# Kernel tuning notes

Measured on AMD Instinct MI355X. Metric: run time of the kernel, lower is better.

## Reference

```python
import jax, jax.numpy as jnp
import numpy as np

N = 50000
E = 800000
IN = 3
H = 64
OUT = 128
L = 4


def _layernorm(x, w, b, eps=1e-5):
    mu = jnp.mean(x, axis=-1, keepdims=True)
    var = jnp.mean(jnp.square(x - mu), axis=-1, keepdims=True)
    return (x - mu) * jax.lax.rsqrt(var + eps) * w + b


def setup_inputs() -> dict:
    key = jax.random.key(0)
    ks = jax.random.split(key, 12)

    def lin(k, fan_in, shape):
        return jax.random.normal(k, shape, dtype=jnp.float32) / np.sqrt(fan_in)

    x = jax.random.normal(ks[0], (N, IN), dtype=jnp.float32)
    edge_index = jax.random.randint(ks[1], (2, E), 0, N, dtype=jnp.int32)
    return {
        "x": x,
        "edge_index": edge_index,
        "in_w": lin(ks[2], IN, (IN, H)), "in_b": jnp.zeros((H,), jnp.float32),
        "ew1": lin(ks[3], 2, (2, H)), "eb1": jnp.zeros((H,), jnp.float32),
        "ew2": lin(ks[4], H, (H, H)), "eb2": jnp.zeros((H,), jnp.float32),
        "cw1": lin(ks[5], H, (L, H, H)), "cb1": jnp.zeros((L, H), jnp.float32),
        "cw2": lin(ks[6], H, (L, H, H)), "cb2": jnp.zeros((L, H), jnp.float32),
        "lnw": jnp.ones((L, H), jnp.float32), "lnb": jnp.zeros((L, H), jnp.float32),
        "fw": lin(ks[7], H, (H, OUT)), "fb": jnp.zeros((OUT,), jnp.float32),
        "rw": lin(ks[8], H, (H, OUT)), "rb": jnp.zeros((OUT,), jnp.float32),
        "ow": jnp.ones((OUT,), jnp.float32), "ob": jnp.zeros((OUT,), jnp.float32),
    }


def reference(x, edge_index, in_w, in_b, ew1, eb1, ew2, eb2,
              cw1, cb1, cw2, cb2, lnw, lnb, fw, fb, rw, rb, ow, ob):
    pos = x[:, :2]
    row, col = edge_index[0], edge_index[1]  # source, target (PyG convention)
    rel_pos = pos[col] - pos[row]                              # [E, 2]
    edge_attr = jnp.maximum(rel_pos @ ew1 + eb1, 0.0) @ ew2 + eb2  # [E, H]

    h = x @ in_w + in_b  # [N, H]
    for i in range(L):
        identity = h
        # GINEConv (eps=0): mlp(x_i + sum_j relu(x_j + e_ij))
        msg = jax.nn.relu(h[row] + edge_attr)                  # [E, H]
        agg = jax.ops.segment_sum(msg, col, num_segments=N)    # [N, H]
        m = h + agg
        m = jnp.maximum(m @ cw1[i] + cb1[i], 0.0) @ cw2[i] + cb2[i]
        m = _layernorm(m, lnw[i], lnb[i])
        h = jax.nn.gelu(m, approximate=False) + identity

    out = (h @ fw + fb) + (h @ rw + rb)
    return _layernorm(out, ow, ob)
```

## Files before the change

kernel.cpp:

```cpp
#include <hip/hip_runtime.h>
#include <hip/hip_fp16.h>
#include <stdint.h>

#define NN 50000
#define NE 800000
#define SCAN_BLOCKS 196

typedef _Float16 half8v __attribute__((ext_vector_type(8)));
typedef float f32x4 __attribute__((ext_vector_type(4)));

static __device__ __forceinline__ __half2 u2h2(unsigned int u) {
    union { unsigned int u; __half2 h; } c; c.u = u; return c.h;
}
static __device__ __forceinline__ unsigned int h22u(__half2 h) {
    union { __half2 h; unsigned int u; } c; c.h = h; return c.u;
}

static __device__ __forceinline__ float4 fma4(float4 a, float s, float4 w) {
    a.x = fmaf(s, w.x, a.x); a.y = fmaf(s, w.y, a.y);
    a.z = fmaf(s, w.z, a.z); a.w = fmaf(s, w.w, a.w);
    return a;
}
static __device__ __forceinline__ void acc8(float* acc, float4 hv, float4 ev) {
    const unsigned int* hu = (const unsigned int*)&hv;
    const unsigned int* eu = (const unsigned int*)&ev;
    #pragma unroll
    for (int q = 0; q < 4; ++q) {
        float2 hf = __half22float2(u2h2(hu[q]));
        float2 ef = __half22float2(u2h2(eu[q]));
        acc[q * 2]     += fmaxf(hf.x + ef.x, 0.f);
        acc[q * 2 + 1] += fmaxf(hf.y + ef.y, 0.f);
    }
}

__global__ __launch_bounds__(256) void k_deg(const int* __restrict__ ei, int* __restrict__ offcur) {
    int e = blockIdx.x * 256 + threadIdx.x;
    atomicAdd(&offcur[ei[NE + e]], 1);
}

__global__ __launch_bounds__(256) void k_scanA(const int* __restrict__ off, int* __restrict__ part) {
    __shared__ int s[256];
    int t = threadIdx.x;
    int idx = blockIdx.x * 256 + t;
    int d = (idx < NN) ? off[idx] : 0;
    s[t] = d; __syncthreads();
    for (int o = 128; o > 0; o >>= 1) {
        if (t < o) s[t] += s[t + o];
        __syncthreads();
    }
    if (t == 0) part[blockIdx.x] = s[0];
}

__global__ __launch_bounds__(256) void k_scanB(int* __restrict__ part) {
    __shared__ int s[256];
    int t = threadIdx.x;
    int d = (t < SCAN_BLOCKS) ? part[t] : 0;
    s[t] = d; __syncthreads();
    #pragma unroll
    for (int o = 1; o < 256; o <<= 1) {
        int v = (t >= o) ? s[t - o] : 0;
        __syncthreads();
        s[t] += v;
        __syncthreads();
    }
    if (t < SCAN_BLOCKS) part[t] = s[t] - d;
}

__global__ __launch_bounds__(256) void k_scanC(int* __restrict__ off, const int* __restrict__ part) {
    __shared__ int s[256];
    int t = threadIdx.x;
    int idx = blockIdx.x * 256 + t;
    int d = (idx < NN) ? off[idx] : 0;
    s[t] = d; __syncthreads();
    #pragma unroll
    for (int o = 1; o < 256; o <<= 1) {
        int v = (t >= o) ? s[t - o] : 0;
        __syncthreads();
        s[t] += v;
        __syncthreads();
    }
    if (idx < NN) off[idx] = s[t] - d + part[blockIdx.x];
}

__global__ __launch_bounds__(256) void k_prep(const float* __restrict__ ew2,
        const float* __restrict__ cw1, const float* __restrict__ cw2,
        __half* __restrict__ wf) {
    int b = blockIdx.x;
    const float* src;
    if (b == 0) src = ew2;
    else {
        int l = (b - 1) >> 1;
        src = ((b - 1) & 1) ? (cw2 + (size_t)l * 4096) : (cw1 + (size_t)l * 4096);
    }
    __half* dst = wf + (size_t)b * 4096;
    int tid = threadIdx.x;
    for (int i = tid; i < 4096; i += 256) {
        int k = i >> 6, n = i & 63;
        int kt = k >> 5, kin = k & 31;
        int quad = kin >> 3, j = kin & 7;
        int nt = n >> 4, nin = n & 15;
        dst[(size_t)((kt * 4 + nt) * 64 + quad * 16 + nin) * 8 + j] = __float2half(src[i]);
    }
}

__global__ __launch_bounds__(256) void k_input(const float* __restrict__ x,
        const float* __restrict__ in_w, const float* __restrict__ in_b,
        __half* __restrict__ Ah) {
    int n = blockIdx.x * 4 + (threadIdx.x >> 6);
    int k = threadIdx.x & 63;
    const float* xr = x + (size_t)n * 3;
    float v = in_b[k] + xr[0] * in_w[k] + xr[1] * in_w[64 + k] + xr[2] * in_w[128 + k];
    Ah[(size_t)n * 64 + k] = __float2half(v);
}

__global__ __launch_bounds__(256) void k_edge(const float* __restrict__ x,
        const int* __restrict__ ei,
        const float* __restrict__ ew1, const float* __restrict__ eb1,
        const float* __restrict__ eb2, const __half* __restrict__ w2f,
        int* __restrict__ offcur, unsigned short* __restrict__ rows,
        __half* __restrict__ ea) {
    __shared__ float s_w1[128], s_b1[64], s_b2[64];
    __shared__ float s_rx[256], s_ry[256];
    __shared__ int s_pos[256];
    __shared__ __half s_d[4][16][80];
    int tid = threadIdx.x, lane = tid & 63, w = tid >> 6;

    half8v bf[8];
    {
        const half8v* W2F = (const half8v*)w2f;
        #pragma unroll
        for (int f = 0; f < 8; ++f) bf[f] = W2F[f * 64 + lane];
    }
    if (tid < 128) s_w1[tid] = ew1[tid];
    if (tid < 64) s_b1[tid] = eb1[tid];
    else if (tid < 128) s_b2[tid - 64] = eb2[tid - 64];
    int eb = blockIdx.x * 256;
    int my_r, my_pos;
    {
        int e = eb + tid;
        int r = ei[e], c = ei[NE + e];
        s_rx[tid] = x[(size_t)c * 3]     - x[(size_t)r * 3];
        s_ry[tid] = x[(size_t)c * 3 + 1] - x[(size_t)r * 3 + 1];
        int pos = atomicAdd(&offcur[c], 1);
        my_r = r; my_pos = pos;
        s_pos[tid] = pos;
    }
    __syncthreads();

    int lm = lane & 15, lq = lane >> 4;
    #pragma unroll
    for (int t = 0; t < 4; ++t) {
        int ebase = w * 64 + t * 16;
        float rx = s_rx[ebase + lm], ry = s_ry[ebase + lm];
        half8v a0, a1;
        #pragma unroll
        for (int j = 0; j < 8; ++j) {
            int k0 = lq * 8 + j;
            a0[j] = (_Float16)fmaxf(fmaf(rx, s_w1[k0], fmaf(ry, s_w1[64 + k0], s_b1[k0])), 0.f);
            int k1 = k0 + 32;
            a1[j] = (_Float16)fmaxf(fmaf(rx, s_w1[k1], fmaf(ry, s_w1[64 + k1], s_b1[k1])), 0.f);
        }
        f32x4 acc[4];
        #pragma unroll
        for (int nt = 0; nt < 4; ++nt) {
            float b = s_b2[nt * 16 + lm];
            acc[nt][0] = b; acc[nt][1] = b; acc[nt][2] = b; acc[nt][3] = b;
            acc[nt] = __builtin_amdgcn_mfma_f32_16x16x32_f16(a0, bf[nt],     acc[nt], 0, 0, 0);
            acc[nt] = __builtin_amdgcn_mfma_f32_16x16x32_f16(a1, bf[4 + nt], acc[nt], 0, 0, 0);
        }
        __builtin_amdgcn_wave_barrier();
        #pragma unroll
        for (int nt = 0; nt < 4; ++nt)
            #pragma unroll
            for (int r = 0; r < 4; ++r)
                s_d[w][lq * 4 + r][nt * 16 + lm] = __float2half(acc[nt][r]);
        __builtin_amdgcn_wave_barrier();
        int row = lane >> 2, seg = lane & 3;
        int pos = s_pos[w * 64 + t * 16 + row];
        uint4 v0 = *(const uint4*)&s_d[w][row][seg * 16];
        uint4 v1 = *(const uint4*)&s_d[w][row][seg * 16 + 8];
        uint4* dst = (uint4*)&ea[(size_t)pos * 64 + seg * 16];
        dst[0] = v0;
        dst[1] = v1;
        __builtin_amdgcn_wave_barrier();
    }
    rows[my_pos] = (unsigned short)my_r;
}

__global__ __launch_bounds__(256) void k_agg(const __half* __restrict__ Ah,
        const __half* __restrict__ ea, const unsigned short* __restrict__ rows,
        const int* __restrict__ offcur, __half* __restrict__ M) {
    const float4* A4 = (const float4*)Ah;
    const float4* E4 = (const float4*)ea;
    int w = threadIdx.x >> 6, lane = threadIdx.x & 63;
    int es = lane >> 3, oc = lane & 7;
    int n = blockIdx.x * 4 + w;
    int p0 = (n == 0) ? 0 : offcur[n - 1];
    int p1 = offcur[n];
    float acc[8] = {0,0,0,0,0,0,0,0};
    float accB[8] = {0,0,0,0,0,0,0,0};
    for (int base = p0; base < p1; base += 64) {
        int cnt = min(64, p1 - base);
        int rl = (int)rows[base + min(lane, cnt - 1)];
        int j = 0;
        for (; j + 16 <= cnt; j += 16) {
            int i0 = j + es, i1 = j + 8 + es;
            int r0 = __shfl(rl, i0, 64);
            int r1 = __shfl(rl, i1, 64);
            float4 h0 = A4[(size_t)r0 * 8 + oc];
            float4 h1 = A4[(size_t)r1 * 8 + oc];
            float4 e0 = E4[(size_t)(base + i0) * 8 + oc];
            float4 e1 = E4[(size_t)(base + i1) * 8 + oc];
            acc8(acc, h0, e0);
            acc8(accB, h1, e1);
        }
        for (; j < cnt; j += 8) {
            int i0 = j + es;
            bool valid = i0 < cnt;
            int ic = valid ? i0 : (cnt - 1);
            int r0 = __shfl(rl, ic, 64);
            float4 h0 = A4[(size_t)r0 * 8 + oc];
            float4 e0 = E4[(size_t)(base + ic) * 8 + oc];
            if (valid) acc8(acc, h0, e0);
        }
    }
    #pragma unroll
    for (int q = 0; q < 8; ++q) acc[q] += accB[q];
    #pragma unroll
    for (int m = 8; m < 64; m <<= 1) {
        #pragma unroll
        for (int q = 0; q < 8; ++q) acc[q] += __shfl_xor(acc[q], m, 64);
    }
    if (es == 0) {
        float4 sv = A4[(size_t)n * 8 + oc];
        const unsigned int* su = (const unsigned int*)&sv;
        unsigned int o[4];
        #pragma unroll
        for (int q = 0; q < 4; ++q) {
            float2 sf = __half22float2(u2h2(su[q]));
            o[q] = h22u(__floats2half2_rn(sf.x + acc[q * 2], sf.y + acc[q * 2 + 1]));
        }
        *(uint4*)&M[(size_t)n * 64 + oc * 8] = *(uint4*)&o[0];
    }
}

__global__ __launch_bounds__(256) void k_node(__half* __restrict__ Ah, const __half* __restrict__ M,
        const __half* __restrict__ w1f, const __half* __restrict__ w2f,
        const float* __restrict__ cb1, const float* __restrict__ cb2,
        const float* __restrict__ lnw, const float* __restrict__ lnb) {
    __shared__ __half s_u[4][16][72];
    __shared__ float s_b1[64], s_b2[64], s_g[64], s_bt[64];
    int tid = threadIdx.x, lane = tid & 63, w = tid >> 6;
    int lm = lane & 15, lq = lane >> 4;

    half8v bw1[8], bw2[8];
    {
        const half8v* W1F = (const half8v*)w1f;
        const half8v* W2F = (const half8v*)w2f;
        #pragma unroll
        for (int f = 0; f < 8; ++f) { bw1[f] = W1F[f * 64 + lane]; bw2[f] = W2F[f * 64 + lane]; }
    }
    if (tid < 64) { s_b1[tid] = cb1[tid]; s_g[tid] = lnw[tid]; }
    else if (tid < 128) { s_b2[tid - 64] = cb2[tid - 64]; s_bt[tid - 64] = lnb[tid - 64]; }
    __syncthreads();

    int nb = blockIdx.x * 64;
    int na = nb + w * 16 + lm;
    int nac = min(na, NN - 1);

    const uint4* M4 = (const uint4*)M;
    uint4 a0u = M4[(size_t)nac * 8 + lq];
    uint4 a1u = M4[(size_t)nac * 8 + 4 + lq];
    half8v a0 = *(const half8v*)&a0u;
    half8v a1 = *(const half8v*)&a1u;

    f32x4 acc[4];
    #pragma unroll
    for (int nt = 0; nt < 4; ++nt) {
        float b = s_b1[nt * 16 + lm];
        acc[nt][0] = b; acc[nt][1] = b; acc[nt][2] = b; acc[nt][3] = b;
        acc[nt] = __builtin_amdgcn_mfma_f32_16x16x32_f16(a0, bw1[nt],     acc[nt], 0, 0, 0);
        acc[nt] = __builtin_amdgcn_mfma_f32_16x16x32_f16(a1, bw1[4 + nt], acc[nt], 0, 0, 0);
    }
    __builtin_amdgcn_wave_barrier();
    #pragma unroll
    for (int nt = 0; nt < 4; ++nt)
        #pragma unroll
        for (int r = 0; r < 4; ++r)
            s_u[w][lq * 4 + r][nt * 16 + lm] = __float2half(fmaxf(acc[nt][r], 0.f));
    __builtin_amdgcn_wave_barrier();

    half8v u0 = *(const half8v*)&s_u[w][lm][lq * 8];
    half8v u1 = *(const half8v*)&s_u[w][lm][32 + lq * 8];
    #pragma unroll
    for (int nt = 0; nt < 4; ++nt) {
        float b = s_b2[nt * 16 + lm];
        acc[nt][0] = b; acc[nt][1] = b; acc[nt][2] = b; acc[nt][3] = b;
        acc[nt] = __builtin_amdgcn_mfma_f32_16x16x32_f16(u0, bw2[nt],     acc[nt], 0, 0, 0);
        acc[nt] = __builtin_amdgcn_mfma_f32_16x16x32_f16(u1, bw2[4 + nt], acc[nt], 0, 0, 0);
    }

    float S[4], SQ[4];
    #pragma unroll
    for (int r = 0; r < 4; ++r) {
        S[r]  = acc[0][r] + acc[1][r] + acc[2][r] + acc[3][r];
        SQ[r] = acc[0][r] * acc[0][r] + acc[1][r] * acc[1][r]
              + acc[2][r] * acc[2][r] + acc[3][r] * acc[3][r];
    }
    #pragma unroll
    for (int m = 1; m < 16; m <<= 1) {
        #pragma unroll
        for (int r = 0; r < 4; ++r) {
            S[r]  += __shfl_xor(S[r], m, 64);
            SQ[r] += __shfl_xor(SQ[r], m, 64);
        }
    }
    __builtin_amdgcn_wave_barrier();
    #pragma unroll
    for (int r = 0; r < 4; ++r) {
        float mu  = S[r] * (1.f / 64.f);
        float var = SQ[r] * (1.f / 64.f) - mu * mu;
        float rs  = rsqrtf(var + 1e-5f);
        #pragma unroll
        for (int nt = 0; nt < 4; ++nt) {
            int c = nt * 16 + lm;
            float y = (acc[nt][r] - mu) * rs * s_g[c] + s_bt[c];
            float ge = 0.5f * y * (1.f + erff(y * 0.70710678118654752f));
            s_u[w][lq * 4 + r][c] = __float2half(ge);
        }
    }
    __builtin_amdgcn_wave_barrier();

    #pragma unroll
    for (int it = 0; it < 2; ++it) {
        int ck = lq + 4 * it;
        int n = nb + w * 16 + lm;
        if (n < NN) {
            uint4 ge8 = *(const uint4*)&s_u[w][lm][ck * 8];
            uint4 id8 = *(const uint4*)&Ah[(size_t)n * 64 + ck * 8];
            const unsigned int* gu = (const unsigned int*)&ge8;
            const unsigned int* iu = (const unsigned int*)&id8;
            unsigned int o[4];
            #pragma unroll
            for (int p = 0; p < 4; ++p) {
                float2 gf = __half22float2(u2h2(gu[p]));
                float2 iff = __half22float2(u2h2(iu[p]));
                o[p] = h22u(__floats2half2_rn(gf.x + iff.x, gf.y + iff.y));
            }
            *(uint4*)&Ah[(size_t)n * 64 + ck * 8] = *(uint4*)&o[0];
        }
    }
}

__global__ __launch_bounds__(256) void k_final(const __half* __restrict__ Ah,
        const float* __restrict__ fw, const float* __restrict__ fb,
        const float* __restrict__ rw, const float* __restrict__ rb,
        const float* __restrict__ ow, const float* __restrict__ ob,
        float* __restrict__ out) {
    __shared__ float s_W[64 * 128];
    __shared__ float s_h[32 * 68];
    __shared__ float s_b[128];
    __shared__ float s_red[32][4];
    int tid = threadIdx.x;
    for (int i = tid; i < 8192; i += 256) s_W[i] = fw[i] + rw[i];
    if (tid < 128) s_b[tid] = fb[tid] + rb[tid];
    int nb = blockIdx.x * 32;
    for (int i = tid; i < 2048; i += 256) {
        int nl = i >> 6, k = i & 63;
        int n = nb + nl;
        s_h[nl * 68 + k] = (n < NN) ? __half2float(Ah[(size_t)n * 64 + k]) : 0.f;
    }
    __syncthreads();

    int lane = tid & 63, w = tid >> 6;
    int chh = w & 1, nh = w >> 1;
    int cq = lane & 15, ng = lane >> 4;
    int c0 = chh * 64 + cq * 4;
    int rbase = nh * 16 + ng * 4;

    float4 acc[4];
    {
        float4 bq = *(const float4*)&s_b[c0];
        acc[0] = bq; acc[1] = bq; acc[2] = bq; acc[3] = bq;
    }
    #pragma unroll 4
    for (int k4 = 0; k4 < 16; ++k4) {
        float4 m0 = *(const float4*)&s_h[(rbase + 0) * 68 + k4 * 4];
        float4 m1 = *(const float4*)&s_h[(rbase + 1) * 68 + k4 * 4];
        float4 m2 = *(const float4*)&s_h[(rbase + 2) * 68 + k4 * 4];
        float4 m3 = *(const float4*)&s_h[(rbase + 3) * 68 + k4 * 4];
        #pragma unroll
        for (int kk = 0; kk < 4; ++kk) {
            float4 w4 = *(const float4*)&s_W[(k4 * 4 + kk) * 128 + c0];
            acc[0] = fma4(acc[0], ((const float*)&m0)[kk], w4);
            acc[1] = fma4(acc[1], ((const float*)&m1)[kk], w4);
            acc[2] = fma4(acc[2], ((const float*)&m2)[kk], w4);
            acc[3] = fma4(acc[3], ((const float*)&m3)[kk], w4);
        }
    }
    #pragma unroll
    for (int j = 0; j < 4; ++j) {
        float4 v = acc[j];
        float sum = v.x + v.y + v.z + v.w;
        float sq  = v.x * v.x + v.y * v.y + v.z * v.z + v.w * v.w;
        #pragma unroll
        for (int m = 1; m < 16; m <<= 1) {
            sum += __shfl_xor(sum, m, 64);
            sq  += __shfl_xor(sq, m, 64);
        }
        if (cq == 0) {
            s_red[rbase + j][chh * 2]     = sum;
            s_red[rbase + j][chh * 2 + 1] = sq;
        }
    }
    __syncthreads();
    float4 gq = *(const float4*)&ow[c0];
    float4 bq = *(const float4*)&ob[c0];
    #pragma unroll
    for (int j = 0; j < 4; ++j) {
        int nl = rbase + j;
        int n = nb + nl;
        float tsum = s_red[nl][0] + s_red[nl][2];
        float tsq  = s_red[nl][1] + s_red[nl][3];
        float mu  = tsum * (1.f / 128.f);
        float var = tsq * (1.f / 128.f) - mu * mu;
        float rs  = rsqrtf(var + 1e-5f);
        if (n < NN) {
            float4 v = acc[j];
            float4 o;
            o.x = (v.x - mu) * rs * gq.x + bq.x;
            o.y = (v.y - mu) * rs * gq.y + bq.y;
            o.z = (v.z - mu) * rs * gq.z + bq.z;
            o.w = (v.w - mu) * rs * gq.w + bq.w;
            *(float4*)&out[(size_t)n * 128 + c0] = o;
        }
    }
}

extern "C" void kernel_launch(void* const* d_in, const int* in_sizes, int n_in,
                              void* d_out, int out_size, void* d_ws, size_t ws_size,
                              hipStream_t stream) {
    const float* x    = (const float*)d_in[0];
    const int*   ei   = (const int*)d_in[1];
    const float* in_w = (const float*)d_in[2];
    const float* in_b = (const float*)d_in[3];
    const float* ew1  = (const float*)d_in[4];
    const float* eb1  = (const float*)d_in[5];
    const float* ew2  = (const float*)d_in[6];
    const float* eb2  = (const float*)d_in[7];
    const float* cw1  = (const float*)d_in[8];
    const float* cb1  = (const float*)d_in[9];
    const float* cw2  = (const float*)d_in[10];
    const float* cb2  = (const float*)d_in[11];
    const float* lnw  = (const float*)d_in[12];
    const float* lnb  = (const float*)d_in[13];
    const float* fw   = (const float*)d_in[14];
    const float* fb   = (const float*)d_in[15];
    const float* rw   = (const float*)d_in[16];
    const float* rb   = (const float*)d_in[17];
    const float* ow   = (const float*)d_in[18];
    const float* ob   = (const float*)d_in[19];
    float* out = (float*)d_out;

    char* ws = (char*)d_ws;
    __half*         ea   = (__half*)ws;
    __half*         Ah   = (__half*)(ws + 102400000);
    unsigned short* rows = (unsigned short*)(ws + 108800000);
    int*            off  = (int*)(ws + 110400000);
    __half*         M    = (__half*)(ws + 110600016);
    __half*         wf   = (__half*)(ws + 117000016);
    int*            part = (int*)M;

    (void)hipMemsetAsync(off, 0, (NN + 1) * sizeof(int), stream);
    k_deg<<<NE / 256, 256, 0, stream>>>(ei, off);
    k_scanA<<<SCAN_BLOCKS, 256, 0, stream>>>(off, part);
    k_scanB<<<1, 256, 0, stream>>>(part);
    k_scanC<<<SCAN_BLOCKS, 256, 0, stream>>>(off, part);
    k_prep<<<9, 256, 0, stream>>>(ew2, cw1, cw2, wf);
    k_input<<<NN / 4, 256, 0, stream>>>(x, in_w, in_b, Ah);
    k_edge<<<NE / 256, 256, 0, stream>>>(x, ei, ew1, eb1, eb2, wf, off, rows, ea);

    const int nodeBlocks = (NN + 63) / 64;
    for (int l = 0; l < 4; ++l) {
        k_agg<<<NN / 4, 256, 0, stream>>>(Ah, ea, rows, off, M);
        k_node<<<nodeBlocks, 256, 0, stream>>>(Ah, M,
            wf + (size_t)(1 + 2 * l) * 4096, wf + (size_t)(2 + 2 * l) * 4096,
            cb1 + (size_t)l * 64, cb2 + (size_t)l * 64,
            lnw + (size_t)l * 64, lnb + (size_t)l * 64);
    }
    k_final<<<(NN + 31) / 32, 256, 0, stream>>>(Ah, fw, fb, rw, rb, ow, ob, out);
}
```

Measured before the change: 406.4 us.

## Recompute edge MLP inside aggregation instead of materializing edge features

Replaces the precomputed 800k×64 fp16 edge-attribute buffer with a compact per-edge record (source row plus fp16 relative position) and recomputes the edge MLP with MFMA inside each aggregation pass. This removes the write of roughly 100 MB of edge features and its re-read in each of the four layers, trading memory traffic for repeated MFMA compute. The aggregation now processes edges in chunks of 16 per wave, with fewer edges in flight per iteration. Storing relative positions in fp16 adds a small precision loss.

```diff
diff --git a/kernel.cpp b/kernel.cpp
--- a/kernel.cpp
+++ b/kernel.cpp
@@ -14,6 +14,12 @@
 }
 static __device__ __forceinline__ unsigned int h22u(__half2 h) {
     union { __half2 h; unsigned int u; } c; c.h = h; return c.u;
+}
+static __device__ __forceinline__ float us2f(unsigned short s) {
+    union { unsigned short s; __half h; } c; c.s = s; return __half2float(c.h);
+}
+static __device__ __forceinline__ unsigned short f2us(float f) {
+    union { __half h; unsigned short s; } c; c.h = __float2half(f); return c.s;
 }
 
 static __device__ __forceinline__ float4 fma4(float4 a, float s, float4 w) {
@@ -113,17 +119,34 @@
     Ah[(size_t)n * 64 + k] = __float2half(v);
 }
 
-__global__ __launch_bounds__(256) void k_edge(const float* __restrict__ x,
-        const int* __restrict__ ei,
+__global__ __launch_bounds__(256) void k_rel(const float* __restrict__ x,
+        const int* __restrict__ ei, int* __restrict__ offcur,
+        ushort4* __restrict__ rec) {
+    int e = blockIdx.x * 256 + threadIdx.x;
+    int r = ei[e], c = ei[NE + e];
+    float rx = x[(size_t)c * 3]     - x[(size_t)r * 3];
+    float ry = x[(size_t)c * 3 + 1] - x[(size_t)r * 3 + 1];
+    int pos = atomicAdd(&offcur[c], 1);
+    ushort4 rc;
+    rc.x = (unsigned short)r;
+    rc.y = f2us(rx);
+    rc.z = f2us(ry);
+    rc.w = 0;
+    rec[pos] = rc;
+}
+
+__global__ __launch_bounds__(256) void k_agg(const __half* __restrict__ Ah,
+        const ushort4* __restrict__ rec, const int* __restrict__ offcur,
+        const __half* __restrict__ w2f,
         const float* __restrict__ ew1, const float* __restrict__ eb1,
-        const float* __restrict__ eb2, const __half* __restrict__ w2f,
-        int* __restrict__ offcur, unsigned short* __restrict__ rows,
-        __half* __restrict__ ea) {
+        const float* __restrict__ eb2,
+        __half* __restrict__ M) {
     __shared__ float s_w1[128], s_b1[64], s_b2[64];
-    __shared__ float s_rx[256], s_ry[256];
-    __shared__ int s_pos[256];
-    __shared__ __half s_d[4][16][80];
+    __shared__ __half s_ea[4][16][80];
+    const float4* A4 = (const float4*)Ah;
     int tid = threadIdx.x, lane = tid & 63, w = tid >> 6;
+    int lm = lane & 15, lq = lane >> 4;
+    int es = lane >> 3, oc = lane & 7;
 
     half8v bf[8];
     {
@@ -134,24 +157,20 @@
     if (tid < 128) s_w1[tid] = ew1[tid];
     if (tid < 64) s_b1[tid] = eb1[tid];
     else if (tid < 128) s_b2[tid - 64] = eb2[tid - 64];
-    int eb = blockIdx.x * 256;
-    int my_r, my_pos;
-    {
-        int e = eb + tid;
-        int r = ei[e], c = ei[NE + e];
-        s_rx[tid] = x[(size_t)c * 3]     - x[(size_t)r * 3];
-        s_ry[tid] = x[(size_t)c * 3 + 1] - x[(size_t)r * 3 + 1];
-        int pos = atomicAdd(&offcur[c], 1);
-        my_r = r; my_pos = pos;
-        s_pos[tid] = pos;
-    }
     __syncthreads();
 
-    int lm = lane & 15, lq = lane >> 4;
-    #pragma unroll
-    for (int t = 0; t < 4; ++t) {
-        int ebase = w * 64 + t * 16;
-        float rx = s_rx[ebase + lm], ry = s_ry[ebase + lm];
+    int n = blockIdx.x * 4 + w;
+    int p0 = (n == 0) ? 0 : offcur[n - 1];
+    int p1 = offcur[n];
+    float acc[8] = {0,0,0,0,0,0,0,0};
+    float accB[8] = {0,0,0,0,0,0,0,0};
+
+    for (int base = p0; base < p1; base += 16) {
+        int cnt = min(16, p1 - base);
+        ushort4 rc = rec[base + min(lm, cnt - 1)];
+        int rl = (int)rc.x;
+        float rx = us2f(rc.y), ry = us2f(rc.z);
+
         half8v a0, a1;
         #pragma unroll
         for (int j = 0; j < 8; ++j) {
@@ -160,69 +179,33 @@
             int k1 = k0 + 32;
             a1[j] = (_Float16)fmaxf(fmaf(rx, s_w1[k1], fmaf(ry, s_w1[64 + k1], s_b1[k1])), 0.f);
         }
-        f32x4 acc[4];
+        f32x4 d[4];
         #pragma unroll
         for (int nt = 0; nt < 4; ++nt) {
             float b = s_b2[nt * 16 + lm];
-            acc[nt][0] = b; acc[nt][1] = b; acc[nt][2] = b; acc[nt][3] = b;
-            acc[nt] = __builtin_amdgcn_mfma_f32_16x16x32_f16(a0, bf[nt],     acc[nt], 0, 0, 0);
-            acc[nt] = __builtin_amdgcn_mfma_f32_16x16x32_f16(a1, bf[4 + nt], acc[nt], 0, 0, 0);
+            d[nt][0] = b; d[nt][1] = b; d[nt][2] = b; d[nt][3] = b;
+            d[nt] = __builtin_amdgcn_mfma_f32_16x16x32_f16(a0, bf[nt],     d[nt], 0, 0, 0);
+            d[nt] = __builtin_amdgcn_mfma_f32_16x16x32_f16(a1, bf[4 + nt], d[nt], 0, 0, 0);
         }
         __builtin_amdgcn_wave_barrier();
         #pragma unroll
         for (int nt = 0; nt < 4; ++nt)
             #pragma unroll
             for (int r = 0; r < 4; ++r)
-                s_d[w][lq * 4 + r][nt * 16 + lm] = __float2half(acc[nt][r]);
+                s_ea[w][lq * 4 + r][nt * 16 + lm] = __float2half(d[nt][r]);
         __builtin_amdgcn_wave_barrier();
-        int row = lane >> 2, seg = lane & 3;
-        int pos = s_pos[w * 64 + t * 16 + row];
-        uint4 v0 = *(const uint4*)&s_d[w][row][seg * 16];
-        uint4 v1 = *(const uint4*)&s_d[w][row][seg * 16 + 8];
-        uint4* dst = (uint4*)&ea[(size_t)pos * 64 + seg * 16];
-        dst[0] = v0;
-        dst[1] = v1;
+
+        int i0 = es, i1 = 8 + es;
+        int ic0 = min(i0, cnt - 1), ic1 = min(i1, cnt - 1);
+        int r0 = __shfl(rl, ic0, 64);
+        int r1 = __shfl(rl, ic1, 64);
+        float4 h0 = A4[(size_t)r0 * 8 + oc];
+        float4 h1 = A4[(size_t)r1 * 8 + oc];
+        float4 e0 = *(const float4*)&s_ea[w][ic0][oc * 8];
+        float4 e1 = *(const float4*)&s_ea[w][ic1][oc * 8];
+        if (i0 < cnt) acc8(acc, h0, e0);
+        if (i1 < cnt) acc8(accB, h1, e1);
         __builtin_amdgcn_wave_barrier();
-    }
-    rows[my_pos] = (unsigned short)my_r;
-}
-
-__global__ __launch_bounds__(256) void k_agg(const __half* __restrict__ Ah,
-        const __half* __restrict__ ea, const unsigned short* __restrict__ rows,
-        const int* __restrict__ offcur, __half* __restrict__ M) {
-    const float4* A4 = (const float4*)Ah;
-    const float4* E4 = (const float4*)ea;
-    int w = threadIdx.x >> 6, lane = threadIdx.x & 63;
-    int es = lane >> 3, oc = lane & 7;
-    int n = blockIdx.x * 4 + w;
-    int p0 = (n == 0) ? 0 : offcur[n - 1];
-    int p1 = offcur[n];
-    float acc[8] = {0,0,0,0,0,0,0,0};
-    float accB[8] = {0,0,0,0,0,0,0,0};
-    for (int base = p0; base < p1; base += 64) {
-        int cnt = min(64, p1 - base);
-        int rl = (int)rows[base + min(lane, cnt - 1)];
-        int j = 0;
-        for (; j + 16 <= cnt; j += 16) {
-            int i0 = j + es, i1 = j + 8 + es;
-            int r0 = __shfl(rl, i0, 64);
-            int r1 = __shfl(rl, i1, 64);
-            float4 h0 = A4[(size_t)r0 * 8 + oc];
-            float4 h1 = A4[(size_t)r1 * 8 + oc];
-            float4 e0 = E4[(size_t)(base + i0) * 8 + oc];
-            float4 e1 = E4[(size_t)(base + i1) * 8 + oc];
-            acc8(acc, h0, e0);
-            acc8(accB, h1, e1);
-        }
-        for (; j < cnt; j += 8) {
-            int i0 = j + es;
-            bool valid = i0 < cnt;
-            int ic = valid ? i0 : (cnt - 1);
-            int r0 = __shfl(rl, ic, 64);
-            float4 h0 = A4[(size_t)r0 * 8 + oc];
-            float4 e0 = E4[(size_t)(base + ic) * 8 + oc];
-            if (valid) acc8(acc, h0, e0);
-        }
     }
     #pragma unroll
     for (int q = 0; q < 8; ++q) acc[q] += accB[q];
@@ -463,12 +446,11 @@
     float* out = (float*)d_out;
 
     char* ws = (char*)d_ws;
-    __half*         ea   = (__half*)ws;
-    __half*         Ah   = (__half*)(ws + 102400000);
-    unsigned short* rows = (unsigned short*)(ws + 108800000);
-    int*            off  = (int*)(ws + 110400000);
-    __half*         M    = (__half*)(ws + 110600016);
-    __half*         wf   = (__half*)(ws + 117000016);
+    ushort4*        rec  = (ushort4*)ws;
+    __half*         Ah   = (__half*)(ws + 6400000);
+    int*            off  = (int*)(ws + 12800000);
+    __half*         M    = (__half*)(ws + 13000016);
+    __half*         wf   = (__half*)(ws + 19400016);
     int*            part = (int*)M;
 
     (void)hipMemsetAsync(off, 0, (NN + 1) * sizeof(int), stream);
@@ -478,11 +460,11 @@
     k_scanC<<<SCAN_BLOCKS, 256, 0, stream>>>(off, part);
     k_prep<<<9, 256, 0, stream>>>(ew2, cw1, cw2, wf);
     k_input<<<NN / 4, 256, 0, stream>>>(x, in_w, in_b, Ah);
-    k_edge<<<NE / 256, 256, 0, stream>>>(x, ei, ew1, eb1, eb2, wf, off, rows, ea);
+    k_rel<<<NE / 256, 256, 0, stream>>>(x, ei, off, rec);
 
     const int nodeBlocks = (NN + 63) / 64;
     for (int l = 0; l < 4; ++l) {
-        k_agg<<<NN / 4, 256, 0, stream>>>(Ah, ea, rows, off, M);
+        k_agg<<<NN / 4, 256, 0, stream>>>(Ah, rec, off, wf, ew1, eb1, eb2, M);
         k_node<<<nodeBlocks, 256, 0, stream>>>(Ah, M,
             wf + (size_t)(1 + 2 * l) * 4096, wf + (size_t)(2 + 2 * l) * 4096,
             cb1 + (size_t)l * 64, cb2 + (size_t)l * 64,
```

Measured after the change: 530.5 us. +30.5%, slower.
